# Optimization experiments

Measured on AMD Instinct MI355X. Metric: run time of the kernel, lower is better.

The kernel has to match this reference:

```python
import jax, jax.numpy as jnp
import numpy as np
import math

D = 256        # embedding_size
NHEAD = 4
HD = D // NHEAD
FF = 2048      # torch TransformerEncoderLayer default dim_feedforward
NLAYER = 3
VOCAB = 30000
OLD = 2048     # resnet50 fc in_features
BPTT = 20
EOS = 2
PAD = 0
MAXLEN = 5000


def make_pe():
    position = np.arange(MAXLEN)[:, None].astype(np.float32)
    div_term = np.exp(np.arange(0, D, 2).astype(np.float32) * (-math.log(10000.0) / D))
    pe = np.zeros((MAXLEN, D), dtype=np.float32)
    pe[:, 0::2] = np.sin(position * div_term)
    pe[:, 1::2] = np.cos(position * div_term)
    return jnp.asarray(pe)  # [maxlen, d]

PE = make_pe()


def setup_inputs() -> dict:
    key = jax.random.key(0)
    ks = jax.random.split(key, 20)
    s = 0.02
    inp = {
        'image_feats': jax.random.normal(ks[0], (64, OLD), jnp.float32),
        'target_ingrs': jax.random.randint(ks[1], (64, BPTT), 0, VOCAB),
        'emb_table': jax.random.normal(ks[2], (VOCAB, D), jnp.float32) * s,
        'W_g2e': jax.random.normal(ks[3], (OLD, D), jnp.float32) * s,
        'b_g2e': jnp.zeros((D,), jnp.float32),
        'W_out': jax.random.normal(ks[4], (D, VOCAB), jnp.float32) * s,
        'b_out': jnp.zeros((VOCAB,), jnp.float32),
    }
    # per-layer transformer params
    Wqkv, bqkv, Wo, bo, W1, b1, W2, b2, g1, be1, g2, be2 = ([] for _ in range(12))
    k = ks[5]
    for l in range(NLAYER):
        k, *sub = jax.random.split(k, 7)
        Wqkv.append(jax.random.normal(sub[0], (D, 3 * D), jnp.float32) * s)
        bqkv.append(jnp.zeros((3 * D,), jnp.float32))
        Wo.append(jax.random.normal(sub[1], (D, D), jnp.float32) * s)
        bo.append(jnp.zeros((D,), jnp.float32))
        W1.append(jax.random.normal(sub[2], (D, FF), jnp.float32) * s)
        b1.append(jnp.zeros((FF,), jnp.float32))
        W2.append(jax.random.normal(sub[3], (FF, D), jnp.float32) * s)
        b2.append(jnp.zeros((D,), jnp.float32))
        g1.append(jnp.ones((D,), jnp.float32)); be1.append(jnp.zeros((D,), jnp.float32))
        g2.append(jnp.ones((D,), jnp.float32)); be2.append(jnp.zeros((D,), jnp.float32))
    stk = lambda xs: jnp.stack(xs)
    inp.update(Wqkv=stk(Wqkv), bqkv=stk(bqkv), Wo=stk(Wo), bo=stk(bo),
               W1=stk(W1), b1=stk(b1), W2=stk(W2), b2=stk(b2),
               g1=stk(g1), be1=stk(be1), g2=stk(g2), be2=stk(be2))
    return inp


def layernorm(x, g, b):
    mu = jnp.mean(x, -1, keepdims=True)
    var = jnp.var(x, -1, keepdims=True)
    return (x - mu) * jax.lax.rsqrt(var + 1e-5) * g + b


def encoder(x, params):
    # x: [S, B, D] (seq-first like torch). Post-norm encoder, ReLU FFN, no mask.
    (Wqkv, bqkv, Wo, bo, W1, b1, W2, b2, g1, be1, g2, be2) = params
    S, B, _ = x.shape
    for l in range(NLAYER):
        qkv = x @ Wqkv[l] + bqkv[l]                  # [S,B,3D]
        q, k, v = jnp.split(qkv, 3, axis=-1)
        def heads(t):  # [S,B,D] -> [B,H,S,hd]
            return t.reshape(S, B, NHEAD, HD).transpose(1, 2, 0, 3)
        q, k, v = heads(q), heads(k), heads(v)
        att = jnp.einsum('bhqd,bhkd->bhqk', q, k) / math.sqrt(HD)
        att = jax.nn.softmax(att, axis=-1)
        o = jnp.einsum('bhqk,bhkd->bhqd', att, v)    # [B,H,S,hd]
        o = o.transpose(2, 0, 1, 3).reshape(S, B, D)
        x = layernorm(x + o @ Wo[l] + bo[l], g1[l], be1[l])
        ff = jax.nn.relu(x @ W1[l] + b1[l]) @ W2[l] + b2[l]
        x = layernorm(x + ff, g2[l], be2[l])
    return x


def mask_from_eos_after(ids):
    # mult_before=False: mask[:,idx] = all(ids[:,1:idx+1] != EOS); mask[:,0]=1
    ne = (ids != EOS)
    ne = ne.at[:, 0].set(True)
    return jnp.cumprod(ne.astype(jnp.int32), axis=1)  # [B,S]


def reference(image_feats, target_ingrs, emb_table, W_g2e, b_g2e, W_out, b_out,
              Wqkv, bqkv, Wo, bo, W1, b1, W2, b2, g1, be1, g2, be2):
    params = (Wqkv, bqkv, Wo, bo, W1, b1, W2, b2, g1, be1, g2, be2)
    B = image_feats.shape[0]
    img_embed = image_feats @ W_g2e + b_g2e          # [B,D]
    bptt = target_ingrs.shape[1]

    # embeds buffer: [bptt, B, D]; position 0 = image embed (note: original code
    # never applies pos_encoder in predict(), so neither do we)
    embeds = jnp.zeros((bptt, B, D), jnp.float32).at[0].set(img_embed)

    probs_steps = []
    words_steps = []
    # loop over decode steps (fixed-length Python loop; each step re-encodes prefix,
    # faithful to original no-KV-cache behavior)
    for i in range(bptt):
        seq = embeds[: i + 1]                        # [i+1, B, D]
        out = encoder(seq, params)[-1]               # [B, D]
        logits = out @ W_out + b_out                 # [B, V]
        sm = jax.nn.softmax(logits, axis=-1)
        widx = jnp.argmax(sm, axis=-1)               # [B]
        probs_steps.append(sm)
        words_steps.append(widx)
        if i + 1 < bptt:
            embeds = embeds.at[i + 1].set(emb_table[widx])

    decoder_out = jnp.stack(probs_steps, axis=1)     # [B, bptt, V]
    sampled_word = jnp.stack(words_steps, axis=1)    # [B, bptt]
    eos = decoder_out[:, :, EOS]
    mask = mask_from_eos_after(target_ingrs)         # [B, bptt] int
    ingr_probs = jnp.max(decoder_out * mask[:, :, None].astype(jnp.float32), axis=1)
    sampled_word = jnp.where(mask == 0, PAD, sampled_word)
    return ingr_probs, sampled_word, eos
```

## Files before the change

### kernel.cpp

```cpp
#include <hip/hip_runtime.h>
#include <math.h>

#define D 256
#define NH 4
#define HDIM 64
#define FFD 2048
#define NL 3
#define VOC 30000
#define BPTT 20
#define BATCH 64
#define NMAX (BPTT*BATCH)
#define NCOLT 118
#define TROWS 32
#define NWG 256
#define NTHR 512

struct Params {
  const float* image_feats; const int* target; const float* emb_table;
  const float* W_g2e; const float* b_g2e;
  const float* W_out; const float* b_out;
  const float* Wqkv; const float* bqkv;
  const float* Wo;   const float* bo;
  const float* W1;   const float* b1;
  const float* W2;   const float* b2;
  const float* g1;   const float* be1;
  const float* g2;   const float* be2;
  float* out_probs; float* out_words; float* out_eos;
  float* embeds; float* xcur; float* xln1; float* qkvb0; float* qkvb;
  float* pp; float* fp; float* logits;
  float* pm; float* pd; float* pv; float* gS;
  int* pi; int* maskS;
  unsigned* flags;
};

__device__ __forceinline__ float cld(const float* p) {
  return __hip_atomic_load(p, __ATOMIC_RELAXED, __HIP_MEMORY_SCOPE_AGENT);
}
__device__ __forceinline__ void cst(float* p, float v) {
  __hip_atomic_store(p, v, __ATOMIC_RELAXED, __HIP_MEMORY_SCOPE_AGENT);
}
__device__ __forceinline__ int cldi(const int* p) {
  return __hip_atomic_load(p, __ATOMIC_RELAXED, __HIP_MEMORY_SCOPE_AGENT);
}
__device__ __forceinline__ void csti(int* p, int v) {
  __hip_atomic_store(p, v, __ATOMIC_RELAXED, __HIP_MEMORY_SCOPE_AGENT);
}
__device__ __forceinline__ float2 cld2(const float* p) {
  unsigned long long u = __hip_atomic_load((const unsigned long long*)p,
                                           __ATOMIC_RELAXED, __HIP_MEMORY_SCOPE_AGENT);
  union { unsigned long long u; float2 f; } x; x.u = u; return x.f;
}
__device__ __forceinline__ void cst2(float* p, float a, float b) {
  union { unsigned long long u; float f[2]; } x; x.f[0] = a; x.f[1] = b;
  __hip_atomic_store((unsigned long long*)p, x.u,
                     __ATOMIC_RELAXED, __HIP_MEMORY_SCOPE_AGENT);
}

__device__ __forceinline__ float wredsum(float s) {
  for (int off = 32; off; off >>= 1) s += __shfl_down(s, off);
  return __shfl(s, 0);
}
__device__ __forceinline__ float wredmax(float m) {
  for (int off = 32; off; off >>= 1) m = fmaxf(m, __shfl_down(m, off));
  return __shfl(m, 0);
}

__device__ __forceinline__ void gbar(unsigned* flags, unsigned epoch) {
  unsigned* rel = flags + NWG*32;
  asm volatile("s_waitcnt vmcnt(0) lgkmcnt(0)" ::: "memory");
  __syncthreads();
  if (blockIdx.x == 0) {
    int ok;
    do {
      int mine = 1;
      if (threadIdx.x > 0 && threadIdx.x < NWG)
        mine = ((int)(__hip_atomic_load(&flags[(unsigned)threadIdx.x * 32u],
                      __ATOMIC_RELAXED, __HIP_MEMORY_SCOPE_AGENT) - epoch) >= 0);
      ok = __syncthreads_and(mine);
      if (!ok) __builtin_amdgcn_s_sleep(1);
    } while (!ok);
    if (threadIdx.x == 0)
      __hip_atomic_store(rel, epoch, __ATOMIC_RELAXED, __HIP_MEMORY_SCOPE_AGENT);
  } else {
    if (threadIdx.x == 0) {
      __hip_atomic_store(&flags[(unsigned)blockIdx.x * 32u], epoch,
                         __ATOMIC_RELAXED, __HIP_MEMORY_SCOPE_AGENT);
      while ((int)(__hip_atomic_load(rel, __ATOMIC_RELAXED,
                   __HIP_MEMORY_SCOPE_AGENT) - epoch) < 0)
        __builtin_amdgcn_s_sleep(2);
    }
    __syncthreads();
  }
  asm volatile("" ::: "memory");
}

__device__ __forceinline__ void stage32(float (*As)[D], const float* src, long row0) {
  for (int idx = threadIdx.x; idx < TROWS*D/2; idx += NTHR) {
    int r = idx >> 7, c2 = (idx & 127)*2;
    float2 v = cld2(src + (row0 + r)*(long)D + c2);
    As[r][c2] = v.x; As[r][c2+1] = v.y;
  }
}

__device__ __forceinline__ void stageLN(float (*As)[D], const float* resid, long row0,
    const float* parts, int nparts, long pstride,
    const float* bias, const float* g, const float* be, float* wr) {
  const int tid = threadIdx.x;
  for (int idx = tid; idx < TROWS*D/2; idx += NTHR) {
    int r = idx >> 7, c2 = (idx & 127)*2;
    long row = row0 + r;
    float2 v = cld2(resid + row*D + c2);
    float vx = v.x + bias[c2], vy = v.y + bias[c2+1];
    for (int q = 0; q < nparts; ++q) {
      float2 pv = cld2(parts + (long)q*pstride + row*D + c2);
      vx += pv.x; vy += pv.y;
    }
    As[r][c2] = vx; As[r][c2+1] = vy;
  }
  __syncthreads();
  const int lane = tid & 63, w = tid >> 6;
#pragma unroll
  for (int j = 0; j < 4; ++j) {
    int r = w*4 + j;
    float4 x = *(float4*)&As[r][lane*4];
    float mu = wredsum(x.x+x.y+x.z+x.w) * (1.f/D);
    float dx = x.x-mu, dy = x.y-mu, dz = x.z-mu, dw = x.w-mu;
    float var = wredsum(dx*dx+dy*dy+dz*dz+dw*dw) * (1.f/D);
    float inv = 1.f/sqrtf(var + 1e-5f);
    float4 gg = *(const float4*)&g[lane*4];
    float4 bb = *(const float4*)&be[lane*4];
    float4 o;
    o.x = dx*inv*gg.x + bb.x; o.y = dy*inv*gg.y + bb.y;
    o.z = dz*inv*gg.z + bb.z; o.w = dw*inv*gg.w + bb.w;
    *(float4*)&As[r][lane*4] = o;
    if (wr) {
      long row = row0 + r;
      cst2(&wr[row*D + lane*4],     o.x, o.y);
      cst2(&wr[row*D + lane*4 + 2], o.z, o.w);
    }
  }
  __syncthreads();
}

__device__ __forceinline__ void mm32w(const float (*As)[D], const float* __restrict__ Wp,
                                      long M, float acc[4][4]) {
  const int r0 = (threadIdx.x >> 6) * 4;
  for (int kk = 0; kk < D; kk += 4) {
    float w[4][4];
#pragma unroll
    for (int q = 0; q < 4; ++q)
      *(float4*)w[q] = *(const float4*)(Wp + (long)(kk+q)*M);
#pragma unroll
    for (int j = 0; j < 4; ++j) {
      float a[4];
      *(float4*)a = *(const float4*)&As[r0+j][kk];
#pragma unroll
      for (int c = 0; c < 4; ++c)
#pragma unroll
        for (int q = 0; q < 4; ++q)
          acc[j][c] += a[q]*w[q][c];
    }
  }
}

__global__ __launch_bounds__(NTHR, 2) void mega(Params p) {
  extern __shared__ char smraw[];
  float (*As)[D] = (float(*)[D])smraw;
  float (*Bs)[D] = (float(*)[D])(smraw + TROWS*D*4);
  float* sm = (float*)smraw;
  const int tid = threadIdx.x, wgid = blockIdx.x;
  const int lane = tid & 63, wave = tid >> 6;
  unsigned ep = 0;
  unsigned* flags = p.flags;

  if (wgid < BATCH) {
    int b = wgid;
    for (int idx = tid; idx < 2048; idx += NTHR) sm[idx] = p.image_feats[b*2048 + idx];
    __syncthreads();
    if (tid < D) {
      float acc = 0.f;
      for (int k = 0; k < 2048; k += 4) {
        float4 xv = *(const float4*)&sm[k];
        acc += xv.x * p.W_g2e[(k+0)*D + tid];
        acc += xv.y * p.W_g2e[(k+1)*D + tid];
        acc += xv.z * p.W_g2e[(k+2)*D + tid];
        acc += xv.w * p.W_g2e[(k+3)*D + tid];
      }
      cst(&p.embeds[(long)b*D + tid], acc + p.b_g2e[tid]);
    }
  }
  gbar(flags, ++ep);

  for (int i = 0; i < BPTT; ++i) {
    const int S = i + 1;

    if (wgid >= NCOLT && wgid < NCOLT + 6) {
      int idx = wgid - NCOLT;
      int tt = idx & 1, cp = idx >> 1;
      long row0 = (long)i*BATCH + tt*TROWS;
      stage32(As, p.embeds, row0);
      __syncthreads();
      float acc[4][4] = {};
      int col = cp*256 + lane*4;
      mm32w(As, p.Wqkv + col, 3*D, acc);
      float bv[4]; *(float4*)bv = *(const float4*)(p.bqkv + col);
      const int r0 = wave*4;
      for (int j = 0; j < 4; ++j) {
        long row = row0 + r0 + j;
        cst2(&p.qkvb0[row*768 + col],     acc[j][0] + bv[0], acc[j][1] + bv[1]);
        cst2(&p.qkvb0[row*768 + col + 2], acc[j][2] + bv[2], acc[j][3] + bv[3]);
      }
    } else if (wgid < NCOLT && i > 0) {
      float* gm = sm; float* ss = sm + 64; int* mk = (int*)(sm + 128);
      if (tid < 64) {
        gm[tid] = cld(&p.gS[tid*2]); ss[tid] = cld(&p.gS[tid*2+1]);
        mk[tid] = cldi(&p.maskS[tid]);
      }
      __syncthreads();
      int cbase = wgid*256;
      for (int idx = tid; idx < BATCH*128; idx += NTHR) {
        int b = idx >> 7, c = cbase + (idx & 127)*2;
        if (c < VOC && (i-1 == 0 || mk[b])) {
          float2 l = cld2(&p.logits[(long)b*VOC + c]);
          float pr0 = expf(l.x - gm[b]) / ss[b];
          float pr1 = expf(l.y - gm[b]) / ss[b];
          float* op = &p.out_probs[(long)b*VOC + c];
          if (i-1 == 0) { op[0] = pr0; op[1] = pr1; }
          else { op[0] = fmaxf(op[0], pr0); op[1] = fmaxf(op[1], pr1); }
        }
      }
    }
    gbar(flags, ++ep);

    for (int l = 0; l < NL; ++l) {
      {
        const float* src = (l == 0) ? p.qkvb0 : p.qkvb;
        float* qs = sm; float* ks = sm + 1280; float* vs = sm + 2560;
        float* ps = sm + 3840;
        int b = wgid & 63, h = wgid >> 6;
        for (int idx = tid; idx < S*32; idx += NTHR) {
          int s = idx >> 5, d2 = (idx & 31)*2;
          long base = (long)(s*BATCH + b)*768 + h*HDIM + d2;
          float2 qv = cld2(&src[base]);
          float2 kv = cld2(&src[base + D]);
          float2 vv = cld2(&src[base + 2*D]);
          qs[s*HDIM+d2] = qv.x; qs[s*HDIM+d2+1] = qv.y;
          ks[s*HDIM+d2] = kv.x; ks[s*HDIM+d2+1] = kv.y;
          vs[s*HDIM+d2] = vv.x; vs[s*HDIM+d2+1] = vv.y;
        }
        __syncthreads();
        const float* Wo2 = p.Wo + (long)l*D*D + (long)h*HDIM*D;
        if (l < NL-1) {
          for (int idx = tid; idx < S*S; idx += NTHR) {
            int si = idx / S, ti = idx - si*S;
            float a = 0.f;
#pragma unroll 8
            for (int k = 0; k < HDIM; ++k) a += qs[si*HDIM+k]*ks[ti*HDIM+k];
            ps[si*(BPTT+1)+ti] = a * 0.125f;
          }
          __syncthreads();
          for (int r = wave; r < S; r += 8) {
            float v = (lane < S) ? ps[r*(BPTT+1)+lane] : -1e30f;
            float m = wredmax(v);
            float e = (lane < S) ? expf(v - m) : 0.f;
            float ssum = wredsum(e);
            if (lane < S) ps[r*(BPTT+1)+lane] = e / ssum;
          }
          __syncthreads();
          for (int idx = tid; idx < S*HDIM; idx += NTHR) {
            int s = idx >> 6, d = idx & 63;
            float a = 0.f;
            for (int t2 = 0; t2 < S; ++t2) a += ps[s*(BPTT+1)+t2]*vs[t2*HDIM+d];
            qs[idx] = a;
          }
          __syncthreads();
          int c0 = lane*4;
          float acc[3][4] = {};
          for (int k = 0; k < HDIM; ++k) {
            float4 w = *(const float4*)&Wo2[(long)k*D + c0];
#pragma unroll
            for (int jj = 0; jj < 3; ++jj) {
              int r = wave + 8*jj;
              float a = (r < S) ? qs[r*HDIM + k] : 0.f;
              acc[jj][0]+=a*w.x; acc[jj][1]+=a*w.y; acc[jj][2]+=a*w.z; acc[jj][3]+=a*w.w;
            }
          }
          for (int jj = 0; jj < 3; ++jj) {
            int r = wave + 8*jj;
            if (r < S) {
              long row = (long)r*BATCH + b;
              cst2(&p.pp[((long)h*NMAX + row)*D + c0],     acc[jj][0], acc[jj][1]);
              cst2(&p.pp[((long)h*NMAX + row)*D + c0 + 2], acc[jj][2], acc[jj][3]);
            }
          }
        } else {
          if (tid < S) {
            float a = 0.f;
            for (int k = 0; k < HDIM; ++k) a += qs[i*HDIM+k]*ks[tid*HDIM+k];
            ps[tid] = a * 0.125f;
          }
          __syncthreads();
          if (wave == 0) {
            float v = (lane < S) ? ps[lane] : -1e30f;
            float m = wredmax(v);
            float e = (lane < S) ? expf(v - m) : 0.f;
            float ssum = wredsum(e);
            if (lane < S) ps[lane] = e / ssum;
          }
          __syncthreads();
          if (tid < HDIM) {
            float a = 0.f;
            for (int t2 = 0; t2 < S; ++t2) a += ps[t2]*vs[t2*HDIM+tid];
            qs[tid] = a;
          }
          __syncthreads();
          if (tid < 128) {
            int c2 = tid*2;
            float a0 = 0.f, a1 = 0.f;
            for (int k = 0; k < HDIM; ++k) {
              a0 += qs[k]*Wo2[(long)k*D + c2];
              a1 += qs[k]*Wo2[(long)k*D + c2 + 1];
            }
            cst2(&p.pp[((long)h*NMAX + (long)i*BATCH + b)*D + c2], a0, a1);
          }
        }
      }
      gbar(flags, ++ep);

      {
        const float* resid = (l == 0) ? p.embeds : p.xcur;
        const float* bol = p.bo + l*D;
        const float* g1l = p.g1 + l*D; const float* be1l = p.be1 + l*D;
        const float* W1l = p.W1 + (long)l*D*FFD;
        const float* b1l = p.b1 + (long)l*FFD;
        const float* W2l = p.W2 + (long)l*FFD*D;
        const int y = wgid & 7, slot = wgid >> 3;
        const int nrt = (l == NL-1) ? 2 : 2*S;
        const long rbase = (l == NL-1) ? (long)i*BATCH : 0;
        for (int tt = slot; tt < nrt; tt += 32) {
          long row0 = rbase + (long)tt*TROWS;
          stageLN(As, resid, row0, p.pp, 4, (long)NMAX*D, bol, g1l, be1l,
                  (y == 0) ? p.xln1 : nullptr);
          float acc1[4][4] = {};
          int fcol = y*256 + lane*4;
          mm32w(As, W1l + fcol, FFD, acc1);
          float bv[4]; *(float4*)bv = *(const float4*)(b1l + fcol);
          const int r0 = wave*4;
          for (int j = 0; j < 4; ++j)
            for (int c = 0; c < 4; ++c)
              Bs[r0+j][lane*4+c] = fmaxf(acc1[j][c] + bv[c], 0.f);
          __syncthreads();
          float acc2[4][4] = {};
          mm32w(Bs, W2l + (long)(y*256)*D + lane*4, D, acc2);
          for (int j = 0; j < 4; ++j) {
            long row = row0 + r0 + j;
            cst2(&p.fp[((long)y*NMAX + row)*D + lane*4],     acc2[j][0], acc2[j][1]);
            cst2(&p.fp[((long)y*NMAX + row)*D + lane*4 + 2], acc2[j][2], acc2[j][3]);
          }
          __syncthreads();
        }
      }
      gbar(flags, ++ep);

      if (l + 1 < NL) {
        const float* b2l = p.b2 + l*D;
        const float* g2l = p.g2 + l*D; const float* be2l = p.be2 + l*D;
        const float* Wl = p.Wqkv + (long)(l+1)*D*768;
        const float* bl = p.bqkv + (long)(l+1)*768;
        for (int t = wgid; t < 6*S; t += NWG) {
          int tt = t % (2*S), cp = t / (2*S);
          long row0 = (long)tt*TROWS;
          stageLN(As, p.xln1, row0, p.fp, 8, (long)NMAX*D, b2l, g2l, be2l,
                  (cp == 0) ? p.xcur : nullptr);
          float acc[4][4] = {};
          int col = cp*256 + lane*4;
          mm32w(As, Wl + col, 768, acc);
          float bv[4]; *(float4*)bv = *(const float4*)(bl + col);
          const int r0 = wave*4;
          for (int j = 0; j < 4; ++j) {
            long row = row0 + r0 + j;
            cst2(&p.qkvb[row*768 + col],     acc[j][0] + bv[0], acc[j][1] + bv[1]);
            cst2(&p.qkvb[row*768 + col + 2], acc[j][2] + bv[2], acc[j][3] + bv[3]);
          }
          __syncthreads();
        }
        gbar(flags, ++ep);
      }
    }

    {
      const float* b2l = p.b2 + (NL-1)*D;
      const float* g2l = p.g2 + (NL-1)*D; const float* be2l = p.be2 + (NL-1)*D;
      const int x = wgid & 7, slot = wgid >> 3;
      const int rowt = slot & 1, cq = slot >> 1;
      const int colt = cq*8 + x;
      if (cq < 15 && colt < NCOLT) {
        long row0 = (long)i*BATCH + rowt*TROWS;
        stageLN(As, p.xln1, row0, p.fp, 8, (long)NMAX*D, b2l, g2l, be2l, nullptr);
        int col = colt*256 + lane*4;
        int colL = col > VOC-4 ? VOC-4 : col;
        float acc[4][4] = {};
        mm32w(As, p.W_out + colL, VOC, acc);
        float bv[4]; *(float4*)bv = *(const float4*)(p.b_out + colL);
        bool valid = (col < VOC);
        const int r0 = wave*4;
        for (int j = 0; j < 4; ++j) {
          int b = rowt*TROWS + r0 + j;
          float v4[4]; float lm = -1e30f;
          for (int c = 0; c < 4; ++c) v4[c] = acc[j][c] + bv[c];
          if (valid) {
            cst2(&p.logits[(long)b*VOC + col],     v4[0], v4[1]);
            cst2(&p.logits[(long)b*VOC + col + 2], v4[2], v4[3]);
            for (int c = 0; c < 4; ++c) lm = fmaxf(lm, v4[c]);
          }
          float m = wredmax(lm);
          float ls = 0.f;
          if (valid) for (int c = 0; c < 4; ++c) ls += expf(v4[c] - m);
          for (int off = 32; off; off >>= 1) ls += __shfl_down(ls, off);
          float av = -1e30f; int ai = VOC;
          if (valid) for (int c = 0; c < 4; ++c) if (v4[c] > av) { av = v4[c]; ai = col + c; }
          for (int off = 32; off; off >>= 1) {
            float av2 = __shfl_down(av, off); int ai2 = __shfl_down(ai, off);
            if (av2 > av || (av2 == av && ai2 < ai)) { av = av2; ai = ai2; }
          }
          if (lane == 0) {
            int pidx = colt*64 + b;
            cst(&p.pm[pidx], m); cst(&p.pd[pidx], ls);
            cst(&p.pv[pidx], av); csti(&p.pi[pidx], ai);
          }
        }
      }
    }
    gbar(flags, ++ep);

    if (wgid < BATCH) {
      int b = wgid;
      float* Lm = sm; float* Ld = sm + 128; float* Lv = sm + 256;
      int* Li = (int*)(sm + 384); int* Lei = Li + 128;
      if (tid < NCOLT) {
        Lm[tid] = cld(&p.pm[tid*64 + b]);
        Ld[tid] = cld(&p.pd[tid*64 + b]);
        Lv[tid] = cld(&p.pv[tid*64 + b]);
        Li[tid] = cldi(&p.pi[tid*64 + b]);
      }
      __syncthreads();
      if (tid == 0) {
        float gmax = -1e30f;
        for (int t2 = 0; t2 < NCOLT; ++t2) gmax = fmaxf(gmax, Lm[t2]);
        float Ssum = 0.f;
        for (int t2 = 0; t2 < NCOLT; ++t2) Ssum += Ld[t2] * expf(Lm[t2] - gmax);
        float bvv = -1e30f; int bi = VOC;
        for (int t2 = 0; t2 < NCOLT; ++t2)
          if (Lv[t2] > bvv || (Lv[t2] == bvv && Li[t2] < bi)) { bvv = Lv[t2]; bi = Li[t2]; }
        int run = 1;
        for (int j = 1; j <= i; ++j) if (p.target[b*BPTT + j] == 2) run = 0;
        float p2 = expf(cld(&p.logits[(long)b*VOC + 2]) - gmax) / Ssum;
        p.out_eos[b*BPTT + i] = p2;
        p.out_words[b*BPTT + i] = run ? (float)bi : 0.f;
        cst(&p.gS[b*2], gmax);
        cst(&p.gS[b*2+1], Ssum);
        csti(&p.maskS[b], run);
        Lei[0] = bi;
      }
      __syncthreads();
      if (i + 1 < BPTT && tid < 128) {
        int ei = Lei[0];
        int c2 = tid*2;
        cst2(&p.embeds[((long)(i+1)*BATCH + b)*D + c2],
             p.emb_table[(long)ei*D + c2], p.emb_table[(long)ei*D + c2 + 1]);
      }
    }
    gbar(flags, ++ep);
  }

  if (wgid < NCOLT) {
    float* gm = sm; float* ss = sm + 64; int* mk = (int*)(sm + 128);
    if (tid < 64) {
      gm[tid] = cld(&p.gS[tid*2]); ss[tid] = cld(&p.gS[tid*2+1]);
      mk[tid] = cldi(&p.maskS[tid]);
    }
    __syncthreads();
    int cbase = wgid*256;
    for (int idx = tid; idx < BATCH*128; idx += NTHR) {
      int b = idx >> 7, c = cbase + (idx & 127)*2;
      if (c < VOC && mk[b]) {
        float2 l = cld2(&p.logits[(long)b*VOC + c]);
        float pr0 = expf(l.x - gm[b]) / ss[b];
        float pr1 = expf(l.y - gm[b]) / ss[b];
        float* op = &p.out_probs[(long)b*VOC + c];
        op[0] = fmaxf(op[0], pr0);
        op[1] = fmaxf(op[1], pr1);
      }
    }
  }
}

extern "C" void kernel_launch(void* const* d_in, const int* in_sizes, int n_in,
                              void* d_out, int out_size, void* d_ws, size_t ws_size,
                              hipStream_t stream) {
  Params P;
  P.image_feats = (const float*)d_in[0];
  P.target      = (const int*)  d_in[1];
  P.emb_table   = (const float*)d_in[2];
  P.W_g2e       = (const float*)d_in[3];
  P.b_g2e       = (const float*)d_in[4];
  P.W_out       = (const float*)d_in[5];
  P.b_out       = (const float*)d_in[6];
  P.Wqkv        = (const float*)d_in[7];
  P.bqkv        = (const float*)d_in[8];
  P.Wo          = (const float*)d_in[9];
  P.bo          = (const float*)d_in[10];
  P.W1          = (const float*)d_in[11];
  P.b1          = (const float*)d_in[12];
  P.W2          = (const float*)d_in[13];
  P.b2          = (const float*)d_in[14];
  P.g1          = (const float*)d_in[15];
  P.be1         = (const float*)d_in[16];
  P.g2          = (const float*)d_in[17];
  P.be2         = (const float*)d_in[18];

  float* out_probs = (float*)d_out;
  P.out_probs = out_probs;
  P.out_words = out_probs + (long)BATCH*VOC;
  P.out_eos   = P.out_words + BATCH*BPTT;

  char* ws = (char*)d_ws;
  P.embeds = (float*)ws;  ws += sizeof(float)*(long)NMAX*D;
  P.xcur   = (float*)ws;  ws += sizeof(float)*(long)NMAX*D;
  P.xln1   = (float*)ws;  ws += sizeof(float)*(long)NMAX*D;
  P.qkvb0  = (float*)ws;  ws += sizeof(float)*(long)NMAX*3*D;
  P.qkvb   = (float*)ws;  ws += sizeof(float)*(long)NMAX*3*D;
  P.pp     = (float*)ws;  ws += sizeof(float)*(long)4*NMAX*D;
  P.fp     = (float*)ws;  ws += sizeof(float)*(long)8*NMAX*D;
  P.logits = (float*)ws;  ws += sizeof(float)*(long)BATCH*VOC;
  P.pm     = (float*)ws;  ws += sizeof(float)*NCOLT*64;
  P.pd     = (float*)ws;  ws += sizeof(float)*NCOLT*64;
  P.pv     = (float*)ws;  ws += sizeof(float)*NCOLT*64;
  P.gS     = (float*)ws;  ws += sizeof(float)*128;
  P.pi     = (int*)ws;    ws += sizeof(int)*NCOLT*64;
  P.maskS  = (int*)ws;    ws += sizeof(int)*64;
  P.flags  = (unsigned*)ws; ws += sizeof(unsigned)*(NWG*32 + 32);

  static bool inited = false;
  if (!inited) {
    hipFuncSetAttribute((const void*)mega,
                        hipFuncAttributeMaxDynamicSharedMemorySize, 65536);
    inited = true;
  }

  hipMemsetAsync(P.flags, 0, sizeof(unsigned)*(NWG*32 + 32), stream);
  void* args[] = { &P };
  hipError_t err = hipLaunchCooperativeKernel((void*)mega, dim3(NWG), dim3(NTHR),
                                              args, 65536, stream);
  if (err != hipSuccess) {
    hipLaunchKernelGGL(mega, dim3(NWG), dim3(NTHR), 65536, stream, P);
  }
}
```

Measured before the change: 9.580 ms.

## Double GEMM row tile to 64 rows so each weight load serves more rows

Raises the row-tile height from 32 to 64 in every fused GEMM stage (QKV, FFN, output projection). Each thread now accumulates 8 rows instead of 4, halving how often weight columns are re-read from global memory per row. The FFN hidden buffer now reuses the As shared buffer instead of a separate Bs, which needs an extra barrier. The cost is half as many work tiles, so fewer workgroups are busy per stage, plus higher register pressure from the 8x4 accumulators.

```diff
diff --git a/kernel.cpp b/kernel.cpp
--- a/kernel.cpp
+++ b/kernel.cpp
@@ -11,7 +11,7 @@
 #define BATCH 64
 #define NMAX (BPTT*BATCH)
 #define NCOLT 118
-#define TROWS 32
+#define TROWS 64
 #define NWG 256
 #define NTHR 512
 
@@ -94,7 +94,7 @@
   asm volatile("" ::: "memory");
 }
 
-__device__ __forceinline__ void stage32(float (*As)[D], const float* src, long row0) {
+__device__ __forceinline__ void stage64(float (*As)[D], const float* src, long row0) {
   for (int idx = threadIdx.x; idx < TROWS*D/2; idx += NTHR) {
     int r = idx >> 7, c2 = (idx & 127)*2;
     float2 v = cld2(src + (row0 + r)*(long)D + c2);
@@ -120,8 +120,8 @@
   __syncthreads();
   const int lane = tid & 63, w = tid >> 6;
 #pragma unroll
-  for (int j = 0; j < 4; ++j) {
-    int r = w*4 + j;
+  for (int j = 0; j < 8; ++j) {
+    int r = w*8 + j;
     float4 x = *(float4*)&As[r][lane*4];
     float mu = wredsum(x.x+x.y+x.z+x.w) * (1.f/D);
     float dx = x.x-mu, dy = x.y-mu, dz = x.z-mu, dw = x.w-mu;
@@ -142,16 +142,16 @@
   __syncthreads();
 }
 
-__device__ __forceinline__ void mm32w(const float (*As)[D], const float* __restrict__ Wp,
-                                      long M, float acc[4][4]) {
-  const int r0 = (threadIdx.x >> 6) * 4;
+__device__ __forceinline__ void mm64(const float (*As)[D], const float* __restrict__ Wp,
+                                     long M, float acc[8][4]) {
+  const int r0 = (threadIdx.x >> 6) * 8;
   for (int kk = 0; kk < D; kk += 4) {
     float w[4][4];
 #pragma unroll
     for (int q = 0; q < 4; ++q)
       *(float4*)w[q] = *(const float4*)(Wp + (long)(kk+q)*M);
 #pragma unroll
-    for (int j = 0; j < 4; ++j) {
+    for (int j = 0; j < 8; ++j) {
       float a[4];
       *(float4*)a = *(const float4*)&As[r0+j][kk];
 #pragma unroll
@@ -166,7 +166,6 @@
 __global__ __launch_bounds__(NTHR, 2) void mega(Params p) {
   extern __shared__ char smraw[];
   float (*As)[D] = (float(*)[D])smraw;
-  float (*Bs)[D] = (float(*)[D])(smraw + TROWS*D*4);
   float* sm = (float*)smraw;
   const int tid = threadIdx.x, wgid = blockIdx.x;
   const int lane = tid & 63, wave = tid >> 6;
@@ -194,18 +193,17 @@
   for (int i = 0; i < BPTT; ++i) {
     const int S = i + 1;
 
-    if (wgid >= NCOLT && wgid < NCOLT + 6) {
-      int idx = wgid - NCOLT;
-      int tt = idx & 1, cp = idx >> 1;
-      long row0 = (long)i*BATCH + tt*TROWS;
-      stage32(As, p.embeds, row0);
+    if (wgid >= NCOLT && wgid < NCOLT + 3) {
+      int cp = wgid - NCOLT;
+      long row0 = (long)i*BATCH;
+      stage64(As, p.embeds, row0);
       __syncthreads();
-      float acc[4][4] = {};
+      float acc[8][4] = {};
       int col = cp*256 + lane*4;
-      mm32w(As, p.Wqkv + col, 3*D, acc);
+      mm64(As, p.Wqkv + col, 3*D, acc);
       float bv[4]; *(float4*)bv = *(const float4*)(p.bqkv + col);
-      const int r0 = wave*4;
-      for (int j = 0; j < 4; ++j) {
+      const int r0 = wave*8;
+      for (int j = 0; j < 8; ++j) {
         long row = row0 + r0 + j;
         cst2(&p.qkvb0[row*768 + col],     acc[j][0] + bv[0], acc[j][1] + bv[1]);
         cst2(&p.qkvb0[row*768 + col + 2], acc[j][2] + bv[2], acc[j][3] + bv[3]);
@@ -335,24 +333,25 @@
         const float* b1l = p.b1 + (long)l*FFD;
         const float* W2l = p.W2 + (long)l*FFD*D;
         const int y = wgid & 7, slot = wgid >> 3;
-        const int nrt = (l == NL-1) ? 2 : 2*S;
+        const int nrt = (l == NL-1) ? 1 : S;
         const long rbase = (l == NL-1) ? (long)i*BATCH : 0;
         for (int tt = slot; tt < nrt; tt += 32) {
           long row0 = rbase + (long)tt*TROWS;
           stageLN(As, resid, row0, p.pp, 4, (long)NMAX*D, bol, g1l, be1l,
                   (y == 0) ? p.xln1 : nullptr);
-          float acc1[4][4] = {};
+          float acc1[8][4] = {};
           int fcol = y*256 + lane*4;
-          mm32w(As, W1l + fcol, FFD, acc1);
+          mm64(As, W1l + fcol, FFD, acc1);
           float bv[4]; *(float4*)bv = *(const float4*)(b1l + fcol);
-          const int r0 = wave*4;
-          for (int j = 0; j < 4; ++j)
+          const int r0 = wave*8;
+          __syncthreads();
+          for (int j = 0; j < 8; ++j)
             for (int c = 0; c < 4; ++c)
-              Bs[r0+j][lane*4+c] = fmaxf(acc1[j][c] + bv[c], 0.f);
-          __syncthreads();
-          float acc2[4][4] = {};
-          mm32w(Bs, W2l + (long)(y*256)*D + lane*4, D, acc2);
-          for (int j = 0; j < 4; ++j) {
+              As[r0+j][lane*4+c] = fmaxf(acc1[j][c] + bv[c], 0.f);
+          __syncthreads();
+          float acc2[8][4] = {};
+          mm64(As, W2l + (long)(y*256)*D + lane*4, D, acc2);
+          for (int j = 0; j < 8; ++j) {
             long row = row0 + r0 + j;
             cst2(&p.fp[((long)y*NMAX + row)*D + lane*4],     acc2[j][0], acc2[j][1]);
             cst2(&p.fp[((long)y*NMAX + row)*D + lane*4 + 2], acc2[j][2], acc2[j][3]);
@@ -367,17 +366,17 @@
         const float* g2l = p.g2 + l*D; const float* be2l = p.be2 + l*D;
         const float* Wl = p.Wqkv + (long)(l+1)*D*768;
         const float* bl = p.bqkv + (long)(l+1)*768;
-        for (int t = wgid; t < 6*S; t += NWG) {
-          int tt = t % (2*S), cp = t / (2*S);
+        for (int t = wgid; t < 3*S; t += NWG) {
+          int tt = t % S, cp = t / S;
           long row0 = (long)tt*TROWS;
           stageLN(As, p.xln1, row0, p.fp, 8, (long)NMAX*D, b2l, g2l, be2l,
                   (cp == 0) ? p.xcur : nullptr);
-          float acc[4][4] = {};
+          float acc[8][4] = {};
           int col = cp*256 + lane*4;
-          mm32w(As, Wl + col, 768, acc);
+          mm64(As, Wl + col, 768, acc);
           float bv[4]; *(float4*)bv = *(const float4*)(bl + col);
-          const int r0 = wave*4;
-          for (int j = 0; j < 4; ++j) {
+          const int r0 = wave*8;
+          for (int j = 0; j < 8; ++j) {
             long row = row0 + r0 + j;
             cst2(&p.qkvb[row*768 + col],     acc[j][0] + bv[0], acc[j][1] + bv[1]);
             cst2(&p.qkvb[row*768 + col + 2], acc[j][2] + bv[2], acc[j][3] + bv[3]);
@@ -391,21 +390,19 @@
     {
       const float* b2l = p.b2 + (NL-1)*D;
       const float* g2l = p.g2 + (NL-1)*D; const float* be2l = p.be2 + (NL-1)*D;
-      const int x = wgid & 7, slot = wgid >> 3;
-      const int rowt = slot & 1, cq = slot >> 1;
-      const int colt = cq*8 + x;
-      if (cq < 15 && colt < NCOLT) {
-        long row0 = (long)i*BATCH + rowt*TROWS;
+      const int colt = wgid;
+      if (colt < NCOLT) {
+        long row0 = (long)i*BATCH;
         stageLN(As, p.xln1, row0, p.fp, 8, (long)NMAX*D, b2l, g2l, be2l, nullptr);
         int col = colt*256 + lane*4;
         int colL = col > VOC-4 ? VOC-4 : col;
-        float acc[4][4] = {};
-        mm32w(As, p.W_out + colL, VOC, acc);
+        float acc[8][4] = {};
+        mm64(As, p.W_out + colL, VOC, acc);
         float bv[4]; *(float4*)bv = *(const float4*)(p.b_out + colL);
         bool valid = (col < VOC);
-        const int r0 = wave*4;
-        for (int j = 0; j < 4; ++j) {
-          int b = rowt*TROWS + r0 + j;
+        const int r0 = wave*8;
+        for (int j = 0; j < 8; ++j) {
+          int b = r0 + j;
           float v4[4]; float lm = -1e30f;
           for (int c = 0; c < 4; ++c) v4[c] = acc[j][c] + bv[c];
           if (valid) {
```

Measured after the change: 12.00 ms. +25.2%, slower.

## Stage weight tiles in shared memory for all block matmuls

Applied to the files above, without the earlier changes.

Replaces the per-wave direct global weight reads in the 32-row matmul helper with cooperative staging of 32x256 weight chunks into LDS. The chunks are then shared by all eight waves. A separate variant handles the clamped output-projection columns. This targets the redundant global/L1 traffic from every wave re-reading the same weight rows. In exchange it adds two block barriers per k-chunk with no double buffering, and raises dynamic shared memory to 96KB, which may limit how many workgroups fit per CU.

```diff
diff --git a/kernel.cpp b/kernel.cpp
--- a/kernel.cpp
+++ b/kernel.cpp
@@ -142,23 +142,65 @@
   __syncthreads();
 }
 
-__device__ __forceinline__ void mm32w(const float (*As)[D], const float* __restrict__ Wp,
-                                      long M, float acc[4][4]) {
+__device__ __forceinline__ void mm32s(const float (*Xs)[D], float (*Ws)[D],
+                                      const float* __restrict__ Wp, long M,
+                                      float acc[4][4]) {
   const int r0 = (threadIdx.x >> 6) * 4;
-  for (int kk = 0; kk < D; kk += 4) {
-    float w[4][4];
-#pragma unroll
-    for (int q = 0; q < 4; ++q)
-      *(float4*)w[q] = *(const float4*)(Wp + (long)(kk+q)*M);
-#pragma unroll
-    for (int j = 0; j < 4; ++j) {
-      float a[4];
-      *(float4*)a = *(const float4*)&As[r0+j][kk];
-#pragma unroll
-      for (int c = 0; c < 4; ++c)
-#pragma unroll
-        for (int q = 0; q < 4; ++q)
-          acc[j][c] += a[q]*w[q][c];
+  const int lane = threadIdx.x & 63;
+  for (int k0 = 0; k0 < D; k0 += 32) {
+    __syncthreads();
+    for (int idx = threadIdx.x; idx < 32*64; idx += NTHR) {
+      int r = idx >> 6, c4 = (idx & 63) * 4;
+      *(float4*)&Ws[r][c4] = *(const float4*)(Wp + (long)(k0 + r)*M + c4);
+    }
+    __syncthreads();
+    for (int kk = 0; kk < 32; kk += 4) {
+      float w[4][4];
+#pragma unroll
+      for (int q = 0; q < 4; ++q)
+        *(float4*)w[q] = *(const float4*)&Ws[kk+q][lane*4];
+#pragma unroll
+      for (int j = 0; j < 4; ++j) {
+        float a[4];
+        *(float4*)a = *(const float4*)&Xs[r0+j][k0+kk];
+#pragma unroll
+        for (int c = 0; c < 4; ++c)
+#pragma unroll
+          for (int q = 0; q < 4; ++q)
+            acc[j][c] += a[q]*w[q][c];
+      }
+    }
+  }
+}
+
+__device__ __forceinline__ void mm32sc(const float (*Xs)[D], float (*Ws)[D],
+                                       const float* __restrict__ Wout, int colt,
+                                       float acc[4][4]) {
+  const int r0 = (threadIdx.x >> 6) * 4;
+  const int lane = threadIdx.x & 63;
+  for (int k0 = 0; k0 < D; k0 += 32) {
+    __syncthreads();
+    for (int idx = threadIdx.x; idx < 32*64; idx += NTHR) {
+      int r = idx >> 6, c4 = (idx & 63) * 4;
+      int eff = colt*256 + c4; if (eff > VOC-4) eff = VOC-4;
+      *(float4*)&Ws[r][c4] = *(const float4*)(Wout + (long)(k0 + r)*VOC + eff);
+    }
+    __syncthreads();
+    for (int kk = 0; kk < 32; kk += 4) {
+      float w[4][4];
+#pragma unroll
+      for (int q = 0; q < 4; ++q)
+        *(float4*)w[q] = *(const float4*)&Ws[kk+q][lane*4];
+#pragma unroll
+      for (int j = 0; j < 4; ++j) {
+        float a[4];
+        *(float4*)a = *(const float4*)&Xs[r0+j][k0+kk];
+#pragma unroll
+        for (int c = 0; c < 4; ++c)
+#pragma unroll
+          for (int q = 0; q < 4; ++q)
+            acc[j][c] += a[q]*w[q][c];
+      }
     }
   }
 }
@@ -166,7 +208,8 @@
 __global__ __launch_bounds__(NTHR, 2) void mega(Params p) {
   extern __shared__ char smraw[];
   float (*As)[D] = (float(*)[D])smraw;
-  float (*Bs)[D] = (float(*)[D])(smraw + TROWS*D*4);
+  float (*Bs)[D] = (float(*)[D])(smraw + 32768);
+  float (*Ws)[D] = (float(*)[D])(smraw + 65536);
   float* sm = (float*)smraw;
   const int tid = threadIdx.x, wgid = blockIdx.x;
   const int lane = tid & 63, wave = tid >> 6;
@@ -202,7 +245,7 @@
       __syncthreads();
       float acc[4][4] = {};
       int col = cp*256 + lane*4;
-      mm32w(As, p.Wqkv + col, 3*D, acc);
+      mm32s(As, Ws, p.Wqkv + cp*256, 3*D, acc);
       float bv[4]; *(float4*)bv = *(const float4*)(p.bqkv + col);
       const int r0 = wave*4;
       for (int j = 0; j < 4; ++j) {
@@ -343,7 +386,7 @@
                   (y == 0) ? p.xln1 : nullptr);
           float acc1[4][4] = {};
           int fcol = y*256 + lane*4;
-          mm32w(As, W1l + fcol, FFD, acc1);
+          mm32s(As, Ws, W1l + y*256, FFD, acc1);
           float bv[4]; *(float4*)bv = *(const float4*)(b1l + fcol);
           const int r0 = wave*4;
           for (int j = 0; j < 4; ++j)
@@ -351,7 +394,7 @@
               Bs[r0+j][lane*4+c] = fmaxf(acc1[j][c] + bv[c], 0.f);
           __syncthreads();
           float acc2[4][4] = {};
-          mm32w(Bs, W2l + (long)(y*256)*D + lane*4, D, acc2);
+          mm32s(Bs, Ws, W2l + (long)(y*256)*D, D, acc2);
           for (int j = 0; j < 4; ++j) {
             long row = row0 + r0 + j;
             cst2(&p.fp[((long)y*NMAX + row)*D + lane*4],     acc2[j][0], acc2[j][1]);
@@ -374,7 +417,7 @@
                   (cp == 0) ? p.xcur : nullptr);
           float acc[4][4] = {};
           int col = cp*256 + lane*4;
-          mm32w(As, Wl + col, 768, acc);
+          mm32s(As, Ws, Wl + cp*256, 768, acc);
           float bv[4]; *(float4*)bv = *(const float4*)(bl + col);
           const int r0 = wave*4;
           for (int j = 0; j < 4; ++j) {
@@ -400,7 +443,7 @@
         int col = colt*256 + lane*4;
         int colL = col > VOC-4 ? VOC-4 : col;
         float acc[4][4] = {};
-        mm32w(As, p.W_out + colL, VOC, acc);
+        mm32sc(As, Ws, p.W_out, colt, acc);
         float bv[4]; *(float4*)bv = *(const float4*)(p.b_out + colL);
         bool valid = (col < VOC);
         const int r0 = wave*4;
@@ -544,15 +587,15 @@
   static bool inited = false;
   if (!inited) {
     hipFuncSetAttribute((const void*)mega,
-                        hipFuncAttributeMaxDynamicSharedMemorySize, 65536);
+                        hipFuncAttributeMaxDynamicSharedMemorySize, 98304);
     inited = true;
   }
 
   hipMemsetAsync(P.flags, 0, sizeof(unsigned)*(NWG*32 + 32), stream);
   void* args[] = { &P };
   hipError_t err = hipLaunchCooperativeKernel((void*)mega, dim3(NWG), dim3(NTHR),
-                                              args, 65536, stream);
+                                              args, 98304, stream);
   if (err != hipSuccess) {
-    hipLaunchKernelGGL(mega, dim3(NWG), dim3(NTHR), 65536, stream, P);
-  }
-}
+    hipLaunchKernelGGL(mega, dim3(NWG), dim3(NTHR), 98304, stream, P);
+  }
+}
```

Result: faster. 9.235 ms (-3.6%).
